# Kernel optimization log

Measured on AMD Instinct MI355X. Metric: run time of the kernel, lower is better.

## Reference

```python
import jax, jax.numpy as jnp
import numpy as np

E = 2048   # embed_dim
H = 16     # num query heads
D = E // H # head_dim = 128
B = 2
S = 2048


def setup_inputs() -> dict:
    key = jax.random.key(0)
    ks = jax.random.split(key, 12)
    sc = 0.02
    return {
        "input": jax.random.normal(ks[0], (B, S, E), jnp.float32),
        "kv": jax.random.normal(ks[1], (B, S, E), jnp.float32),
        "Wq": jax.random.normal(ks[2], (E, E), jnp.float32) * sc,
        "bq": jnp.zeros((E,), jnp.float32),
        "Wk": jax.random.normal(ks[3], (D, E), jnp.float32) * sc,
        "bk": jnp.zeros((D,), jnp.float32),
        "Wv": jax.random.normal(ks[4], (D, E), jnp.float32) * sc,
        "bv": jnp.zeros((D,), jnp.float32),
        "Wo": jax.random.normal(ks[5], (E, E), jnp.float32) * sc,
        "bo": jnp.zeros((E,), jnp.float32),
        "expanding_context": 0,
    }


def reference(input, kv, Wq, bq, Wk, bk, Wv, bv, Wo, bo, expanding_context):
    b, s, _ = input.shape
    # projections (torch Linear: x @ W.T + b)
    q = (input @ Wq.T + bq).reshape(b, s, H, D).transpose(0, 2, 1, 3)  # [B,H,S,D]
    k = kv @ Wk.T + bk  # [B,S,D] single KV head
    v = kv @ Wv.T + bv  # [B,S,D]
    # scores with single KV head broadcast across query heads
    scores = jnp.einsum('bhsd,btd->bhst', q, k) / jnp.sqrt(jnp.float32(D))
    causal = jnp.triu(jnp.ones((s, s), bool), k=1)  # True above diagonal
    scores = jnp.where(causal[None, None], jnp.float32(-jnp.inf), scores)
    attn = jax.nn.softmax(scores, axis=-1)
    out = jnp.einsum('bhst,btd->bhsd', attn, v)  # [B,H,S,D]
    out = out.transpose(0, 2, 1, 3).reshape(b, s, E)
    return out @ Wo.T + bo
```

## Files before the change

### kernel.cpp

```cpp
#include <hip/hip_runtime.h>

#define B_  2
#define S_  2048
#define E_  2048
#define H_  16
#define D_  128
#define BS_ (B_*S_)

typedef __bf16 bf16_t;
typedef __bf16 bf16x8 __attribute__((ext_vector_type(8)));
typedef __bf16 bf16x4 __attribute__((ext_vector_type(4)));
typedef float  f32x4  __attribute__((ext_vector_type(4)));

#define QSCALE 0.1275174131003543f

__device__ __forceinline__ void gld16(const bf16_t* g, bf16_t* l) {
    __builtin_amdgcn_global_load_lds(
        (const __attribute__((address_space(1))) void*)g,
        (__attribute__((address_space(3))) void*)l,
        16, 0, 0);
}

__global__ void cvt_all(const float* __restrict__ s0, const float* __restrict__ s1,
                        const float* __restrict__ s2, const float* __restrict__ s3,
                        const float* __restrict__ s4, const float* __restrict__ s5,
                        bf16_t* d0, bf16_t* d1, bf16_t* d2,
                        bf16_t* d3, bf16_t* d4, bf16_t* d5)
{
    long i = ((long)blockIdx.x * blockDim.x + threadIdx.x) * 4;
    const float* s; bf16_t* d;
    if      (i <  8388608) { s = s0; d = d0; }
    else if (i < 16777216) { s = s1; d = d1; i -=  8388608; }
    else if (i < 20971520) { s = s2; d = d2; i -= 16777216; }
    else if (i < 21233664) { s = s3; d = d3; i -= 20971520; }
    else if (i < 21495808) { s = s4; d = d4; i -= 21233664; }
    else                   { s = s5; d = d5; i -= 21495808; }
    float4 v = *(const float4*)(s + i);
    bf16x4 o;
    o[0] = (bf16_t)v.x; o[1] = (bf16_t)v.y; o[2] = (bf16_t)v.z; o[3] = (bf16_t)v.w;
    *(bf16x4*)(d + i) = o;
}

template<int EP>
__device__ __forceinline__ void gemm_tile64(
    const bf16_t* __restrict__ A, const bf16_t* __restrict__ W,
    const float* __restrict__ biasA, const float* __restrict__ biasB,
    float* __restrict__ Cf, bf16_t* __restrict__ Cb,
    int N, int K, float scale, int m0, int w_n0, int c_n0,
    bf16_t* As, bf16_t* Bs)
{
    const int tid  = threadIdx.x;
    const int wave = tid >> 6, lane = tid & 63;
    const int wm = wave >> 1, wn = wave & 1;
    const int lrow = lane & 15, quad = lane >> 4;
    const int r8 = lane >> 3, c8 = (lane & 7) << 3;

    f32x4 acc[4][2] = {};

    for (int k0 = 0; k0 < K; k0 += 64) {
        __syncthreads();
#pragma unroll
        for (int j = 0; j < 4; ++j) {
            int base = (wave * 4 + j) * 8;
            gld16(A + (size_t)(m0 + base + r8) * K + k0 + c8, &As[base * 64]);
        }
#pragma unroll
        for (int j = 0; j < 2; ++j) {
            int base = (wave * 2 + j) * 8;
            gld16(W + (size_t)(w_n0 + base + r8) * K + k0 + c8, &Bs[base * 64]);
        }
        __syncthreads();
#pragma unroll
        for (int ks = 0; ks < 2; ++ks) {
            bf16x8 af[4], bfr[2];
#pragma unroll
            for (int mt = 0; mt < 4; ++mt)
                af[mt] = *(const bf16x8*)&As[(wm * 64 + mt * 16 + lrow) * 64 + ks * 32 + quad * 8];
#pragma unroll
            for (int nt = 0; nt < 2; ++nt)
                bfr[nt] = *(const bf16x8*)&Bs[(wn * 32 + nt * 16 + lrow) * 64 + ks * 32 + quad * 8];
#pragma unroll
            for (int mt = 0; mt < 4; ++mt)
#pragma unroll
                for (int nt = 0; nt < 2; ++nt)
                    acc[mt][nt] = __builtin_amdgcn_mfma_f32_16x16x32_bf16(
                        af[mt], bfr[nt], acc[mt][nt], 0, 0, 0);
        }
    }

#pragma unroll
    for (int mt = 0; mt < 4; ++mt) {
#pragma unroll
        for (int nt = 0; nt < 2; ++nt) {
            int nn = wn * 32 + nt * 16 + lrow;
            int col = c_n0 + nn;
            float bvv = (EP == 1 && biasB && col >= 128) ? biasB[col - 128]
                                                         : biasA[col];
#pragma unroll
            for (int r = 0; r < 4; ++r) {
                int row = m0 + wm * 64 + mt * 16 + quad * 4 + r;
                float v = (acc[mt][nt][r] + bvv) * scale;
                if (EP == 0) Cf[(size_t)row * N + col] = v;
                else         Cb[(size_t)row * N + col] = (bf16_t)v;
            }
        }
    }
}

__global__ __launch_bounds__(256) void gemm_qkv(
    const bf16_t* __restrict__ xb, const bf16_t* __restrict__ kvb,
    const bf16_t* __restrict__ Wq, const bf16_t* __restrict__ Wkv,
    const float* __restrict__ bq, const float* __restrict__ bk,
    const float* __restrict__ bv,
    bf16_t* __restrict__ Qb, bf16_t* __restrict__ KVb)
{
    __shared__ __align__(16) bf16_t As[128 * 64];
    __shared__ __align__(16) bf16_t Bs[64 * 64];
    const int m0 = blockIdx.y * 128;
    if (blockIdx.x < 32) {
        int n0 = blockIdx.x * 64;
        gemm_tile64<1>(xb, Wq, bq, nullptr, nullptr, Qb, E_, E_, QSCALE,
                       m0, n0, n0, As, Bs);
    } else {
        int n0 = (blockIdx.x - 32) * 64;
        gemm_tile64<1>(kvb, Wkv, bk, bv, nullptr, KVb, 256, E_, 1.0f,
                       m0, n0, n0, As, Bs);
    }
}

__global__ __launch_bounds__(256) void gemm_o(
    const bf16_t* __restrict__ A, const bf16_t* __restrict__ W,
    const float* __restrict__ bias, float* __restrict__ Cf)
{
    __shared__ __align__(16) bf16_t As[128 * 64];
    __shared__ __align__(16) bf16_t Bs[64 * 64];
    int n0 = blockIdx.x * 64;
    gemm_tile64<0>(A, W, bias, nullptr, Cf, nullptr, E_, E_, 1.0f,
                   blockIdx.y * 128, n0, n0, As, Bs);
}

__global__ __launch_bounds__(512, 4) void mqa_attn(
    const bf16_t* __restrict__ Q, const bf16_t* __restrict__ KV,
    bf16_t* __restrict__ O)
{
    __shared__ __align__(16) bf16_t Kt[64][136];
    __shared__ __align__(16) bf16_t Vt[128][72];
    __shared__ __align__(16) bf16_t Pl[8][16][72];

    const int bx = blockIdx.x, h = blockIdx.y, b = blockIdx.z;
    const int qb = b ? bx : (15 - bx);
    const int tid = threadIdx.x, wave = tid >> 6, lane = tid & 63;
    const int lrow = lane & 15, quad = lane >> 4;
    const int q0 = qb * 128 + wave * 16;

    const bf16_t* kvp = KV + (size_t)(b * S_) * 256;

    bf16x8 qf[4];
    {
        const bf16_t* qp = Q + ((size_t)(b * S_ + q0 + lrow)) * E_ + h * D_ + quad * 8;
#pragma unroll
        for (int ks = 0; ks < 4; ++ks) qf[ks] = *(const bf16x8*)(qp + ks * 32);
    }

    f32x4 oacc[8] = {};
    float rs[4] = {0.f, 0.f, 0.f, 0.f};

    const int ntiles = 2 * qb + 2;
    bf16x8 kreg[2], vreg[2];

#pragma unroll
    for (int i = 0; i < 2; ++i) {
        int c = tid + 512 * i;
        kreg[i] = *(const bf16x8*)(kvp + (size_t)(c >> 4) * 256 + ((c & 15) << 3));
        vreg[i] = *(const bf16x8*)(kvp + (size_t)(c & 63) * 256 + 128 + ((c >> 6) << 3));
    }

    for (int kt = 0; kt < ntiles; ++kt) {
        const int k_base = kt * 64;
        __syncthreads();
#pragma unroll
        for (int i = 0; i < 2; ++i) {
            int c = tid + 512 * i;
            *(bf16x8*)&Kt[c >> 4][(c & 15) << 3] = kreg[i];
            int n = c & 63, d0 = (c >> 6) << 3;
#pragma unroll
            for (int j = 0; j < 8; ++j) Vt[d0 + j][n] = vreg[i][j];
        }
        __syncthreads();
        if (kt + 1 < ntiles) {
            const int nb = (kt + 1) * 64;
#pragma unroll
            for (int i = 0; i < 2; ++i) {
                int c = tid + 512 * i;
                kreg[i] = *(const bf16x8*)(kvp + (size_t)(nb + (c >> 4)) * 256 + ((c & 15) << 3));
                vreg[i] = *(const bf16x8*)(kvp + (size_t)(nb + (c & 63)) * 256 + 128 + ((c >> 6) << 3));
            }
        }

        if (k_base <= q0 + 15) {
            f32x4 sc[4] = {};
#pragma unroll
            for (int ks = 0; ks < 4; ++ks) {
                bf16x8 a = qf[ks];
#pragma unroll
                for (int c = 0; c < 4; ++c) {
                    bf16x8 kb = *(const bf16x8*)&Kt[c * 16 + lrow][ks * 32 + quad * 8];
                    sc[c] = __builtin_amdgcn_mfma_f32_16x16x32_bf16(a, kb, sc[c], 0, 0, 0);
                }
            }
            const bool diag = (k_base + 63 > q0);
#pragma unroll
            for (int c = 0; c < 4; ++c) {
#pragma unroll
                for (int r = 0; r < 4; ++r) {
                    float s = sc[c][r];
                    if (diag) {
                        int kj = k_base + c * 16 + lrow;
                        int qi = q0 + quad * 4 + r;
                        if (kj > qi) s = -1e30f;
                    }
                    float p = exp2f(fminf(s, 110.f));
                    rs[r] += p;
                    Pl[wave][quad * 4 + r][c * 16 + lrow] = (bf16_t)p;
                }
            }
#pragma unroll
            for (int ks = 0; ks < 2; ++ks) {
                bf16x8 ap = *(const bf16x8*)&Pl[wave][lrow][ks * 32 + quad * 8];
#pragma unroll
                for (int dt = 0; dt < 8; ++dt) {
                    bf16x8 bv = *(const bf16x8*)&Vt[dt * 16 + lrow][ks * 32 + quad * 8];
                    oacc[dt] = __builtin_amdgcn_mfma_f32_16x16x32_bf16(ap, bv, oacc[dt], 0, 0, 0);
                }
            }
        }
    }

#pragma unroll
    for (int off = 8; off >= 1; off >>= 1)
#pragma unroll
        for (int r = 0; r < 4; ++r) rs[r] += __shfl_xor(rs[r], off, 16);
#pragma unroll
    for (int r = 0; r < 4; ++r) {
        float inv = 1.0f / rs[r];
        int row = q0 + quad * 4 + r;
#pragma unroll
        for (int dt = 0; dt < 8; ++dt)
            O[((size_t)(b * S_ + row)) * E_ + h * D_ + dt * 16 + lrow] =
                (bf16_t)(oacc[dt][r] * inv);
    }
}

extern "C" void kernel_launch(void* const* d_in, const int* in_sizes, int n_in,
                              void* d_out, int out_size, void* d_ws, size_t ws_size,
                              hipStream_t stream)
{
    const float* x   = (const float*)d_in[0];
    const float* kv  = (const float*)d_in[1];
    const float* Wq  = (const float*)d_in[2];
    const float* bq  = (const float*)d_in[3];
    const float* Wk  = (const float*)d_in[4];
    const float* bk  = (const float*)d_in[5];
    const float* Wv  = (const float*)d_in[6];
    const float* bv  = (const float*)d_in[7];
    const float* Wo  = (const float*)d_in[8];
    const float* bo  = (const float*)d_in[9];
    float* out = (float*)d_out;

    bf16_t* p    = (bf16_t*)d_ws;
    bf16_t* xb   = p;  p += (size_t)BS_ * E_;
    bf16_t* kvb  = p;  p += (size_t)BS_ * E_;
    bf16_t* Wqb  = p;  p += (size_t)E_ * E_;
    bf16_t* Wkvb = p;  p += (size_t)2 * D_ * E_;
    bf16_t* Wob  = p;  p += (size_t)E_ * E_;
    bf16_t* Qb   = p;  p += (size_t)BS_ * E_;
    bf16_t* KVb  = p;  p += (size_t)BS_ * 256;
    bf16_t* Ob   = p;  p += (size_t)BS_ * E_;

    cvt_all<<<dim3(25088), dim3(256), 0, stream>>>(
        x, kv, Wq, Wk, Wv, Wo,
        xb, kvb, Wqb, Wkvb, Wkvb + (size_t)D_ * E_, Wob);

    gemm_qkv<<<dim3(36, BS_ / 128), 256, 0, stream>>>(
        xb, kvb, Wqb, Wkvb, bq, bk, bv, Qb, KVb);

    mqa_attn<<<dim3(S_ / 128, H_, B_), 512, 0, stream>>>(Qb, KVb, Ob);

    gemm_o<<<dim3(E_ / 64, BS_ / 128), 256, 0, stream>>>(Ob, Wob, bo, out);
}
```

Measured before the change: 362.5 us.

## Restructure GEMMs with register-held A and double-buffered B; widen attention waves

The GEMM core now tiles 256x64 per block. Each wave loads its 64 rows of A straight from global memory into registers, and only the shared W tile is staged in LDS, double-buffered so the next K slice loads while the current one is computed. The attention kernel drops to 256 threads, with each wave handling 32 query rows (two MFMA row tiles) so every K/V fragment read from LDS feeds twice as many MFMAs. This is meant to cut LDS traffic and barrier overhead and raise the MFMA-to-load ratio. The cost is higher register pressure, fewer blocks in the GEMMs, and uncoalesced, non-LDS A loads from global memory.

```diff
diff --git a/kernel.cpp b/kernel.cpp
--- a/kernel.cpp
+++ b/kernel.cpp
@@ -42,63 +42,77 @@
 }
 
 template<int EP>
-__device__ __forceinline__ void gemm_tile64(
+__device__ __forceinline__ void gemm_core(
     const bf16_t* __restrict__ A, const bf16_t* __restrict__ W,
     const float* __restrict__ biasA, const float* __restrict__ biasB,
     float* __restrict__ Cf, bf16_t* __restrict__ Cb,
-    int N, int K, float scale, int m0, int w_n0, int c_n0,
-    bf16_t* As, bf16_t* Bs)
+    int N, float scale, int m0_blk, int w_n0, int c_n0,
+    bf16_t* Bs)
 {
     const int tid  = threadIdx.x;
     const int wave = tid >> 6, lane = tid & 63;
-    const int wm = wave >> 1, wn = wave & 1;
     const int lrow = lane & 15, quad = lane >> 4;
     const int r8 = lane >> 3, c8 = (lane & 7) << 3;
-
-    f32x4 acc[4][2] = {};
-
-    for (int k0 = 0; k0 < K; k0 += 64) {
-        __syncthreads();
-#pragma unroll
-        for (int j = 0; j < 4; ++j) {
-            int base = (wave * 4 + j) * 8;
-            gld16(A + (size_t)(m0 + base + r8) * K + k0 + c8, &As[base * 64]);
-        }
+    const int m0 = m0_blk + wave * 64;
+    const bf16_t* Arow = A + (size_t)(m0 + lrow) * 2048;
+
+    bf16x8 a0[4][2], a1[4][2];
+    f32x4 acc[4][4] = {};
+
+    auto loadA = [&](bf16x8 (&ar)[4][2], int k0) {
+#pragma unroll
+        for (int mt = 0; mt < 4; ++mt)
+#pragma unroll
+            for (int ks = 0; ks < 2; ++ks)
+                ar[mt][ks] = *(const bf16x8*)(Arow + (size_t)mt * 16 * 2048
+                                              + k0 + ks * 32 + quad * 8);
+    };
+    auto stageB = [&](int k0, int buf) {
 #pragma unroll
         for (int j = 0; j < 2; ++j) {
             int base = (wave * 2 + j) * 8;
-            gld16(W + (size_t)(w_n0 + base + r8) * K + k0 + c8, &Bs[base * 64]);
-        }
+            gld16(W + (size_t)(w_n0 + base + r8) * 2048 + k0 + c8,
+                  &Bs[buf * 4096 + base * 64]);
+        }
+    };
+    auto compute = [&](bf16x8 (&ar)[4][2], int buf) {
+        const bf16_t* Bc = Bs + buf * 4096;
+#pragma unroll
+        for (int ks = 0; ks < 2; ++ks) {
+            bf16x8 bfr[4];
+#pragma unroll
+            for (int nt = 0; nt < 4; ++nt)
+                bfr[nt] = *(const bf16x8*)&Bc[(nt * 16 + lrow) * 64 + ks * 32 + quad * 8];
+#pragma unroll
+            for (int mt = 0; mt < 4; ++mt)
+#pragma unroll
+                for (int nt = 0; nt < 4; ++nt)
+                    acc[mt][nt] = __builtin_amdgcn_mfma_f32_16x16x32_bf16(
+                        ar[mt][ks], bfr[nt], acc[mt][nt], 0, 0, 0);
+        }
+    };
+
+    loadA(a0, 0);
+    stageB(0, 0);
+    for (int ki = 0; ki < 32; ki += 2) {
         __syncthreads();
-#pragma unroll
-        for (int ks = 0; ks < 2; ++ks) {
-            bf16x8 af[4], bfr[2];
-#pragma unroll
-            for (int mt = 0; mt < 4; ++mt)
-                af[mt] = *(const bf16x8*)&As[(wm * 64 + mt * 16 + lrow) * 64 + ks * 32 + quad * 8];
-#pragma unroll
-            for (int nt = 0; nt < 2; ++nt)
-                bfr[nt] = *(const bf16x8*)&Bs[(wn * 32 + nt * 16 + lrow) * 64 + ks * 32 + quad * 8];
-#pragma unroll
-            for (int mt = 0; mt < 4; ++mt)
-#pragma unroll
-                for (int nt = 0; nt < 2; ++nt)
-                    acc[mt][nt] = __builtin_amdgcn_mfma_f32_16x16x32_bf16(
-                        af[mt], bfr[nt], acc[mt][nt], 0, 0, 0);
-        }
+        if (ki + 1 < 32) { stageB((ki + 1) << 6, 1); loadA(a1, (ki + 1) << 6); }
+        compute(a0, 0);
+        __syncthreads();
+        if (ki + 2 < 32) { stageB((ki + 2) << 6, 0); loadA(a0, (ki + 2) << 6); }
+        compute(a1, 1);
     }
 
 #pragma unroll
     for (int mt = 0; mt < 4; ++mt) {
 #pragma unroll
-        for (int nt = 0; nt < 2; ++nt) {
-            int nn = wn * 32 + nt * 16 + lrow;
+        for (int nt = 0; nt < 4; ++nt) {
+            int nn = nt * 16 + lrow;
             int col = c_n0 + nn;
-            float bvv = (EP == 1 && biasB && col >= 128) ? biasB[col - 128]
-                                                         : biasA[col];
+            float bvv = (biasB && col >= 128) ? biasB[col - 128] : biasA[col];
 #pragma unroll
             for (int r = 0; r < 4; ++r) {
-                int row = m0 + wm * 64 + mt * 16 + quad * 4 + r;
+                int row = m0 + mt * 16 + quad * 4 + r;
                 float v = (acc[mt][nt][r] + bvv) * scale;
                 if (EP == 0) Cf[(size_t)row * N + col] = v;
                 else         Cb[(size_t)row * N + col] = (bf16_t)v;
@@ -107,70 +121,68 @@
     }
 }
 
-__global__ __launch_bounds__(256) void gemm_qkv(
+__global__ __launch_bounds__(256, 2) void gemm_qkv(
     const bf16_t* __restrict__ xb, const bf16_t* __restrict__ kvb,
     const bf16_t* __restrict__ Wq, const bf16_t* __restrict__ Wkv,
     const float* __restrict__ bq, const float* __restrict__ bk,
     const float* __restrict__ bv,
     bf16_t* __restrict__ Qb, bf16_t* __restrict__ KVb)
 {
-    __shared__ __align__(16) bf16_t As[128 * 64];
-    __shared__ __align__(16) bf16_t Bs[64 * 64];
-    const int m0 = blockIdx.y * 128;
+    __shared__ __align__(16) bf16_t Bs[2 * 4096];
+    const int m0 = blockIdx.y * 256;
     if (blockIdx.x < 32) {
         int n0 = blockIdx.x * 64;
-        gemm_tile64<1>(xb, Wq, bq, nullptr, nullptr, Qb, E_, E_, QSCALE,
-                       m0, n0, n0, As, Bs);
+        gemm_core<1>(xb, Wq, bq, nullptr, nullptr, Qb, E_, QSCALE, m0, n0, n0, Bs);
     } else {
         int n0 = (blockIdx.x - 32) * 64;
-        gemm_tile64<1>(kvb, Wkv, bk, bv, nullptr, KVb, 256, E_, 1.0f,
-                       m0, n0, n0, As, Bs);
-    }
-}
-
-__global__ __launch_bounds__(256) void gemm_o(
+        gemm_core<1>(kvb, Wkv, bk, bv, nullptr, KVb, 256, 1.0f, m0, n0, n0, Bs);
+    }
+}
+
+__global__ __launch_bounds__(256, 2) void gemm_o(
     const bf16_t* __restrict__ A, const bf16_t* __restrict__ W,
     const float* __restrict__ bias, float* __restrict__ Cf)
 {
-    __shared__ __align__(16) bf16_t As[128 * 64];
-    __shared__ __align__(16) bf16_t Bs[64 * 64];
+    __shared__ __align__(16) bf16_t Bs[2 * 4096];
     int n0 = blockIdx.x * 64;
-    gemm_tile64<0>(A, W, bias, nullptr, Cf, nullptr, E_, E_, 1.0f,
-                   blockIdx.y * 128, n0, n0, As, Bs);
-}
-
-__global__ __launch_bounds__(512, 4) void mqa_attn(
+    gemm_core<0>(A, W, bias, nullptr, Cf, nullptr, E_, 1.0f,
+                 blockIdx.y * 256, n0, n0, Bs);
+}
+
+__global__ __launch_bounds__(256, 2) void mqa_attn(
     const bf16_t* __restrict__ Q, const bf16_t* __restrict__ KV,
     bf16_t* __restrict__ O)
 {
     __shared__ __align__(16) bf16_t Kt[64][136];
     __shared__ __align__(16) bf16_t Vt[128][72];
-    __shared__ __align__(16) bf16_t Pl[8][16][72];
+    __shared__ __align__(16) bf16_t Pl[4][32][72];
 
     const int bx = blockIdx.x, h = blockIdx.y, b = blockIdx.z;
     const int qb = b ? bx : (15 - bx);
     const int tid = threadIdx.x, wave = tid >> 6, lane = tid & 63;
     const int lrow = lane & 15, quad = lane >> 4;
-    const int q0 = qb * 128 + wave * 16;
+    const int q0 = qb * 128 + wave * 32;
 
     const bf16_t* kvp = KV + (size_t)(b * S_) * 256;
 
-    bf16x8 qf[4];
-    {
-        const bf16_t* qp = Q + ((size_t)(b * S_ + q0 + lrow)) * E_ + h * D_ + quad * 8;
-#pragma unroll
-        for (int ks = 0; ks < 4; ++ks) qf[ks] = *(const bf16x8*)(qp + ks * 32);
-    }
-
-    f32x4 oacc[8] = {};
-    float rs[4] = {0.f, 0.f, 0.f, 0.f};
+    bf16x8 qf[2][4];
+#pragma unroll
+    for (int mt = 0; mt < 2; ++mt) {
+        const bf16_t* qp = Q + ((size_t)(b * S_ + q0 + mt * 16 + lrow)) * E_
+                           + h * D_ + quad * 8;
+#pragma unroll
+        for (int ks = 0; ks < 4; ++ks) qf[mt][ks] = *(const bf16x8*)(qp + ks * 32);
+    }
+
+    f32x4 oacc[2][8] = {};
+    float rs[2][4] = {};
 
     const int ntiles = 2 * qb + 2;
-    bf16x8 kreg[2], vreg[2];
-
-#pragma unroll
-    for (int i = 0; i < 2; ++i) {
-        int c = tid + 512 * i;
+    bf16x8 kreg[4], vreg[4];
+
+#pragma unroll
+    for (int i = 0; i < 4; ++i) {
+        int c = tid + 256 * i;
         kreg[i] = *(const bf16x8*)(kvp + (size_t)(c >> 4) * 256 + ((c & 15) << 3));
         vreg[i] = *(const bf16x8*)(kvp + (size_t)(c & 63) * 256 + 128 + ((c >> 6) << 3));
     }
@@ -179,8 +191,8 @@
         const int k_base = kt * 64;
         __syncthreads();
 #pragma unroll
-        for (int i = 0; i < 2; ++i) {
-            int c = tid + 512 * i;
+        for (int i = 0; i < 4; ++i) {
+            int c = tid + 256 * i;
             *(bf16x8*)&Kt[c >> 4][(c & 15) << 3] = kreg[i];
             int n = c & 63, d0 = (c >> 6) << 3;
 #pragma unroll
@@ -190,64 +202,72 @@
         if (kt + 1 < ntiles) {
             const int nb = (kt + 1) * 64;
 #pragma unroll
-            for (int i = 0; i < 2; ++i) {
-                int c = tid + 512 * i;
+            for (int i = 0; i < 4; ++i) {
+                int c = tid + 256 * i;
                 kreg[i] = *(const bf16x8*)(kvp + (size_t)(nb + (c >> 4)) * 256 + ((c & 15) << 3));
                 vreg[i] = *(const bf16x8*)(kvp + (size_t)(nb + (c & 63)) * 256 + 128 + ((c >> 6) << 3));
             }
         }
 
-        if (k_base <= q0 + 15) {
-            f32x4 sc[4] = {};
+        if (k_base <= q0 + 31) {
+            f32x4 sc[2][4] = {};
 #pragma unroll
             for (int ks = 0; ks < 4; ++ks) {
-                bf16x8 a = qf[ks];
 #pragma unroll
                 for (int c = 0; c < 4; ++c) {
                     bf16x8 kb = *(const bf16x8*)&Kt[c * 16 + lrow][ks * 32 + quad * 8];
-                    sc[c] = __builtin_amdgcn_mfma_f32_16x16x32_bf16(a, kb, sc[c], 0, 0, 0);
+                    sc[0][c] = __builtin_amdgcn_mfma_f32_16x16x32_bf16(qf[0][ks], kb, sc[0][c], 0, 0, 0);
+                    sc[1][c] = __builtin_amdgcn_mfma_f32_16x16x32_bf16(qf[1][ks], kb, sc[1][c], 0, 0, 0);
                 }
             }
             const bool diag = (k_base + 63 > q0);
 #pragma unroll
-            for (int c = 0; c < 4; ++c) {
-#pragma unroll
-                for (int r = 0; r < 4; ++r) {
-                    float s = sc[c][r];
-                    if (diag) {
-                        int kj = k_base + c * 16 + lrow;
-                        int qi = q0 + quad * 4 + r;
-                        if (kj > qi) s = -1e30f;
+            for (int mt = 0; mt < 2; ++mt) {
+#pragma unroll
+                for (int c = 0; c < 4; ++c) {
+#pragma unroll
+                    for (int r = 0; r < 4; ++r) {
+                        float s = sc[mt][c][r];
+                        if (diag) {
+                            int kj = k_base + c * 16 + lrow;
+                            int qi = q0 + mt * 16 + quad * 4 + r;
+                            if (kj > qi) s = -1e30f;
+                        }
+                        float p = exp2f(fminf(s, 110.f));
+                        rs[mt][r] += p;
+                        Pl[wave][mt * 16 + quad * 4 + r][c * 16 + lrow] = (bf16_t)p;
                     }
-                    float p = exp2f(fminf(s, 110.f));
-                    rs[r] += p;
-                    Pl[wave][quad * 4 + r][c * 16 + lrow] = (bf16_t)p;
                 }
             }
 #pragma unroll
             for (int ks = 0; ks < 2; ++ks) {
-                bf16x8 ap = *(const bf16x8*)&Pl[wave][lrow][ks * 32 + quad * 8];
+                bf16x8 ap0 = *(const bf16x8*)&Pl[wave][lrow][ks * 32 + quad * 8];
+                bf16x8 ap1 = *(const bf16x8*)&Pl[wave][16 + lrow][ks * 32 + quad * 8];
 #pragma unroll
                 for (int dt = 0; dt < 8; ++dt) {
                     bf16x8 bv = *(const bf16x8*)&Vt[dt * 16 + lrow][ks * 32 + quad * 8];
-                    oacc[dt] = __builtin_amdgcn_mfma_f32_16x16x32_bf16(ap, bv, oacc[dt], 0, 0, 0);
+                    oacc[0][dt] = __builtin_amdgcn_mfma_f32_16x16x32_bf16(ap0, bv, oacc[0][dt], 0, 0, 0);
+                    oacc[1][dt] = __builtin_amdgcn_mfma_f32_16x16x32_bf16(ap1, bv, oacc[1][dt], 0, 0, 0);
                 }
             }
         }
     }
 
 #pragma unroll
-    for (int off = 8; off >= 1; off >>= 1)
-#pragma unroll
-        for (int r = 0; r < 4; ++r) rs[r] += __shfl_xor(rs[r], off, 16);
-#pragma unroll
-    for (int r = 0; r < 4; ++r) {
-        float inv = 1.0f / rs[r];
-        int row = q0 + quad * 4 + r;
-#pragma unroll
-        for (int dt = 0; dt < 8; ++dt)
-            O[((size_t)(b * S_ + row)) * E_ + h * D_ + dt * 16 + lrow] =
-                (bf16_t)(oacc[dt][r] * inv);
+    for (int mt = 0; mt < 2; ++mt) {
+#pragma unroll
+        for (int off = 8; off >= 1; off >>= 1)
+#pragma unroll
+            for (int r = 0; r < 4; ++r) rs[mt][r] += __shfl_xor(rs[mt][r], off, 16);
+#pragma unroll
+        for (int r = 0; r < 4; ++r) {
+            float inv = 1.0f / rs[mt][r];
+            int row = q0 + mt * 16 + quad * 4 + r;
+#pragma unroll
+            for (int dt = 0; dt < 8; ++dt)
+                O[((size_t)(b * S_ + row)) * E_ + h * D_ + dt * 16 + lrow] =
+                    (bf16_t)(oacc[mt][dt][r] * inv);
+        }
     }
 }
 
@@ -281,10 +301,10 @@
         x, kv, Wq, Wk, Wv, Wo,
         xb, kvb, Wqb, Wkvb, Wkvb + (size_t)D_ * E_, Wob);
 
-    gemm_qkv<<<dim3(36, BS_ / 128), 256, 0, stream>>>(
+    gemm_qkv<<<dim3(36, BS_ / 256), 256, 0, stream>>>(
         xb, kvb, Wqb, Wkvb, bq, bk, bv, Qb, KVb);
 
-    mqa_attn<<<dim3(S_ / 128, H_, B_), 512, 0, stream>>>(Qb, KVb, Ob);
-
-    gemm_o<<<dim3(E_ / 64, BS_ / 128), 256, 0, stream>>>(Ob, Wob, bo, out);
-}
+    mqa_attn<<<dim3(S_ / 128, H_, B_), 256, 0, stream>>>(Qb, KVb, Ob);
+
+    gemm_o<<<dim3(E_ / 64, BS_ / 256), 256, 0, stream>>>(Ob, Wob, bo, out);
+}
```

After: 462.3 us. +27.5%, slower.
